# Performance work log

Hardware: AMD Instinct MI355X
Metric: run time of the kernel (lower is better)

## Reference

```python
import jax, jax.numpy as jnp
import numpy as np

B, N, D = 1024, 32, 512  # graphs, node types (=nodes per graph), node_dim
EPS = 1e-5

def setup_inputs() -> dict:
    key = jax.random.key(0)
    ks = jax.random.split(key, 6)
    z = jax.random.normal(ks[0], (B, N, D), jnp.float32)
    # each graph contains every node type exactly once, in random order
    idx = jax.vmap(lambda k: jax.random.permutation(k, N))(jax.random.split(ks[1], B)).astype(jnp.int32)
    A = jax.random.normal(ks[2], (N, N), jnp.float32) / np.sqrt(N)
    W1 = jax.random.normal(ks[3], (N, D, 2 * D), jnp.float32) / np.sqrt(D)
    b1 = jnp.zeros((N, 2 * D), jnp.float32)
    W2 = jax.random.normal(ks[4], (N, 2 * D, D), jnp.float32) / np.sqrt(2 * D)
    b2 = jnp.zeros((N, D), jnp.float32)
    gamma = jnp.ones((D,), jnp.float32)
    beta = jnp.zeros((D,), jnp.float32)
    return dict(z=z, idx=idx, A=A, W1=W1, b1=b1, W2=W2, b2=b2, gamma=gamma, beta=beta)

def _layernorm(x, g, b):
    m = jnp.mean(x, axis=-1, keepdims=True)
    v = jnp.var(x, axis=-1, keepdims=True)
    return (x - m) * jax.lax.rsqrt(v + EPS) * g + b

def reference(z, idx, A, W1, b1, W2, b2, gamma, beta):
    # per-graph submatrix of global A: A_sub[b] = A[node_index, node_index]
    A_sub = A[idx[:, :, None], idx[:, None, :]]            # [B,K,K]
    # Az[b] = A_sub[b].T @ z[b]
    Az = jnp.einsum('bkj,bkd->bjd', A_sub, z)              # [B,K,D]
    Az = _layernorm(Az, gamma, beta)
    # route node of type t to expert t: inv[b,t] = position of type t in graph b
    inv = jnp.argsort(idx, axis=1)                         # [B,N]
    x = jnp.take_along_axis(Az, inv[:, :, None], axis=1)   # [B,N,D] type-ordered
    # per-type 2-layer MLP experts (Linear -> ELU -> Linear), dropout in eval mode
    h = jax.nn.elu(jnp.einsum('bnd,ndh->bnh', x, W1) + b1) # [B,N,2D]
    y = jnp.einsum('bnh,nhd->bnd', h, W2) + b2             # [B,N,D]
    # scatter back to node order: node j in graph b has type idx[b,j]
    mix = jnp.take_along_axis(y, idx[:, :, None].astype(jnp.int32), axis=1)
    return mix + Az
```

## Files before the change

kernel.cpp:

```cpp
#include <hip/hip_runtime.h>
#include <hip/hip_bf16.h>
#include <math.h>

#define B_  1024
#define N_  32
#define D_  512
#define EPS_ 1e-5f

typedef __attribute__((ext_vector_type(8))) short bf16x8;
typedef __attribute__((ext_vector_type(4))) float f32x4;
using bf16 = __hip_bfloat16;
typedef unsigned int u32;
typedef const u32 __attribute__((address_space(1)))* gp_t;
typedef u32 __attribute__((address_space(3)))* sp_t;

static __device__ __forceinline__ void gload16(const void* g, void* s) {
  __builtin_amdgcn_global_load_lds((gp_t)g, (sp_t)s, 16, 0, 0);
}
static __device__ __forceinline__ void bar() {
  asm volatile("s_barrier" ::: "memory");
}

static __device__ __forceinline__ unsigned short f2bf(float f) {
  union { float f; u32 u; } c; c.f = f;
  u32 r = c.u + 0x7fff + ((c.u >> 16) & 1);
  return (unsigned short)(r >> 16);
}
static __device__ __forceinline__ float bf2f(unsigned short h) {
  union { u32 u; float f; } c; c.u = ((u32)h) << 16;
  return c.f;
}

static __device__ __forceinline__ void transpose_tile(
    const float* __restrict__ in, bf16* __restrict__ out,
    int R, int C, int bx, int by, int bz, int t) {
  __shared__ unsigned short tile[64][65];
  const size_t mat = (size_t)bz * (size_t)R * (size_t)C;
  const float* inp = in + mat;
  bf16* outp = out + mat;
  const int c0 = bx * 64, r0 = by * 64;
  const int tr = t >> 4;
  const int tc = (t & 15) * 4;
#pragma unroll
  for (int i = 0; i < 4; ++i) {
    const int r = tr + i * 16;
    float4 v = *(const float4*)&inp[(size_t)(r0 + r) * C + c0 + tc];
    tile[r][tc + 0] = f2bf(v.x);
    tile[r][tc + 1] = f2bf(v.y);
    tile[r][tc + 2] = f2bf(v.z);
    tile[r][tc + 3] = f2bf(v.w);
  }
  __syncthreads();
#pragma unroll
  for (int i = 0; i < 2; ++i) {
    const int chunk = i * 256 + t;
    const int c = chunk >> 3, r8 = (chunk & 7) * 8;
    union { bf16x8 v; unsigned short u[8]; } pk;
#pragma unroll
    for (int k = 0; k < 8; ++k) pk.u[k] = tile[r8 + k][c];
    *(bf16x8*)&outp[(size_t)(c0 + c) * R + r0 + r8] = pk.v;
  }
}

static __device__ __forceinline__ void mix_ln_body(
    int b, int t,
    const float* __restrict__ z, const int* __restrict__ idx,
    const float* __restrict__ A, const float* __restrict__ gamma,
    const float* __restrict__ beta, bf16* __restrict__ x_ws,
    int* __restrict__ inv_ws) {
  __shared__ float As[32][32];
  __shared__ int   p[32];
  __shared__ float red1[4][32];
  __shared__ float red2[4][32];
  __shared__ float meanS[32];
  __shared__ float rstdS[32];

  const int lane = t & 63, wid = t >> 6;
  const int llo = lane & 15, lhi = lane >> 4;

  if (t < 32) {
    int v = idx[b * 32 + t];
    p[t] = v;
    inv_ws[b * 32 + v] = t;
  }
  __syncthreads();
#pragma unroll
  for (int i = 0; i < 4; ++i) {
    const int id = i * 256 + t;
    As[id >> 5][id & 31] = A[p[id >> 5] * 32 + (id & 31)];
  }
  __syncthreads();

  bf16x8 af[2];
#pragma unroll
  for (int nt = 0; nt < 2; ++nt) {
    union { bf16x8 v; unsigned short s[8]; } u;
#pragma unroll
    for (int j = 0; j < 8; ++j)
      u.s[j] = f2bf(As[lhi * 8 + j][nt * 16 + llo]);
    af[nt] = u.v;
  }

  const float* zb = z + (size_t)b * (N_ * D_) + (size_t)(lhi * 8) * D_ + llo;
  const f32x4 fz = {0.f, 0.f, 0.f, 0.f};
  f32x4 acc[2][8];
#pragma unroll
  for (int nt = 0; nt < 2; ++nt)
#pragma unroll
    for (int dt = 0; dt < 8; ++dt) acc[nt][dt] = fz;

#pragma unroll
  for (int h = 0; h < 2; ++h) {
    float zr[4][8];
#pragma unroll
    for (int dd = 0; dd < 4; ++dd)
#pragma unroll
      for (int j = 0; j < 8; ++j)
        zr[dd][j] = zb[j * D_ + ((wid * 8 + h * 4 + dd) * 16)];
#pragma unroll
    for (int dd = 0; dd < 4; ++dd) {
      const int dt = h * 4 + dd;
      union { bf16x8 v; unsigned short s[8]; } u;
#pragma unroll
      for (int j = 0; j < 8; ++j) u.s[j] = f2bf(zr[dd][j]);
      acc[0][dt] = __builtin_amdgcn_mfma_f32_16x16x32_bf16(af[0], u.v, acc[0][dt], 0, 0, 0);
      acc[1][dt] = __builtin_amdgcn_mfma_f32_16x16x32_bf16(af[1], u.v, acc[1][dt], 0, 0, 0);
    }
  }

  float s1[2][4], s2[2][4];
#pragma unroll
  for (int nt = 0; nt < 2; ++nt)
#pragma unroll
    for (int r = 0; r < 4; ++r) {
      float a = 0.f, q = 0.f;
#pragma unroll
      for (int dt = 0; dt < 8; ++dt) {
        float v = acc[nt][dt][r];
        a += v; q += v * v;
      }
#pragma unroll
      for (int mk = 1; mk < 16; mk <<= 1) {
        a += __shfl_xor(a, mk);
        q += __shfl_xor(q, mk);
      }
      s1[nt][r] = a; s2[nt][r] = q;
    }
  if (llo == 0) {
#pragma unroll
    for (int nt = 0; nt < 2; ++nt)
#pragma unroll
      for (int r = 0; r < 4; ++r) {
        const int n = nt * 16 + lhi * 4 + r;
        red1[wid][n] = s1[nt][r];
        red2[wid][n] = s2[nt][r];
      }
  }
  __syncthreads();
  if (t < 32) {
    float S1 = red1[0][t] + red1[1][t] + red1[2][t] + red1[3][t];
    float S2 = red2[0][t] + red2[1][t] + red2[2][t] + red2[3][t];
    float mean = S1 * (1.f / D_);
    float var  = S2 * (1.f / D_) - mean * mean;
    meanS[t] = mean;
    rstdS[t] = rsqrtf(var + EPS_);
  }
  __syncthreads();

  float gv[8], bev[8];
#pragma unroll
  for (int dt = 0; dt < 8; ++dt) {
    const int d = (wid * 8 + dt) * 16 + llo;
    gv[dt] = gamma[d]; bev[dt] = beta[d];
  }
#pragma unroll
  for (int nt = 0; nt < 2; ++nt)
#pragma unroll
    for (int r = 0; r < 4; ++r) {
      const int n = nt * 16 + lhi * 4 + r;
      const float mn = meanS[n], rs = rstdS[n];
      unsigned short* xrow = (unsigned short*)(x_ws + ((size_t)n * B_ + b) * D_);
#pragma unroll
      for (int dt = 0; dt < 8; ++dt) {
        const int d = (wid * 8 + dt) * 16 + llo;
        float v = (acc[nt][dt][r] - mn) * rs * gv[dt] + bev[dt];
        xrow[d] = f2bf(v);
      }
    }
}

__global__ __launch_bounds__(256) void prep_kernel(
    const float* __restrict__ W1, const float* __restrict__ W2,
    bf16* __restrict__ W1t, bf16* __restrict__ W2t,
    const float* __restrict__ z, const int* __restrict__ idx,
    const float* __restrict__ A, const float* __restrict__ gamma,
    const float* __restrict__ beta, bf16* __restrict__ x_ws,
    int* __restrict__ inv_ws) {
  const int bid = blockIdx.x;
  const int t = threadIdx.x;
  if (bid < 4096) {
    transpose_tile(W1, W1t, 512, 1024, bid & 15, (bid >> 4) & 7, bid >> 7, t);
  } else if (bid < 8192) {
    const int b2 = bid - 4096;
    transpose_tile(W2, W2t, 1024, 512, b2 & 7, (b2 >> 3) & 15, b2 >> 7, t);
  } else {
    mix_ln_body(bid - 8192, t, z, idx, A, gamma, beta, x_ws, inv_ws);
  }
}

#define STGA(P, H, S)                                                         \
  gload16(Ag + (size_t)((H) * 128) * KD + (S) * 32 + soff,                    \
          lds + (P) * 16384 + (H) * 8192 + dof)
#define STGB(P, H, S)                                                         \
  gload16(Bg + (size_t)((H) * 128) * KD + (S) * 32 + soff,                    \
          lds + 32768 + (P) * 16384 + (H) * 8192 + dof)

#define RDA(P, H, AV) do {                                                    \
    const char* a_ = lds + (P) * 16384 + (H) * 8192;                          \
    AV[0] = *(const bf16x8*)(a_ + (widA * 32 + llo) * 64 + kx);               \
    AV[1] = *(const bf16x8*)(a_ + (widA * 32 + 16 + llo) * 64 + kx);          \
  } while (0)
#define RDB(P, H, BV) do {                                                    \
    const char* b_ = lds + 32768 + (P) * 16384 + (H) * 8192;                  \
    _Pragma("unroll")                                                         \
    for (int fj = 0; fj < 4; ++fj)                                            \
      BV[fj] = *(const bf16x8*)(b_ + (widB * 64 + fj * 16 + llo) * 64 + kx);  \
  } while (0)

#define MMA8(QR, QC, AV, BV) do {                                             \
    __builtin_amdgcn_s_setprio(1);                                            \
    _Pragma("unroll")                                                         \
    for (int fi = 0; fi < 2; ++fi)                                            \
      _Pragma("unroll")                                                       \
      for (int fj = 0; fj < 4; ++fj)                                          \
        acc[QR][QC][fi][fj] = __builtin_amdgcn_mfma_f32_16x16x32_bf16(        \
            AV[fi], BV[fj], acc[QR][QC][fi][fj], 0, 0, 0);                    \
    __builtin_amdgcn_s_setprio(0);                                            \
  } while (0)

#define VMC0() asm volatile("s_waitcnt vmcnt(0)" ::: "memory")

#define SUBTILE(P, S) do {                                                    \
    bf16x8 av[2], bv0[4], bv1[4];                                             \
    RDA(P, 0, av); RDB(P, 0, bv0); RDB(P, 1, bv1);                            \
    MMA8(0, 0, av, bv0);                                                      \
    MMA8(0, 1, av, bv1);                                                      \
    RDA(P, 1, av);                                                            \
    MMA8(1, 0, av, bv0);                                                      \
    MMA8(1, 1, av, bv1);                                                      \
    VMC0();                                  \
    bar();                                  \
    if ((S) + 2 < NS) {                                                       \
      STGA(P, 0, (S) + 2); STGA(P, 1, (S) + 2);                               \
      STGB(P, 0, (S) + 2); STGB(P, 1, (S) + 2);                               \
    }                                                                         \
  } while (0)

template <int KD, int NS>
static __device__ __forceinline__ void gemm_core(
    const bf16* __restrict__ Ag, const bf16* __restrict__ Bg,
    char* __restrict__ lds, f32x4 (&acc)[2][2][2][4], const int t) {
  const int lane = t & 63, wid = t >> 6;
  const int llo = lane & 15, lhi = lane >> 4;
  const int widA = wid & 3, widB = wid >> 2;
  const int kx = (lhi ^ ((llo >> 1) & 3)) * 16;
  const size_t soff = (size_t)(t >> 2) * KD + (size_t)(((t & 3) ^ ((t >> 3) & 3))) * 8;
  const int dof = wid * 1024;

  STGA(0, 0, 0); STGA(0, 1, 0); STGB(0, 0, 0); STGB(0, 1, 0);
  STGA(1, 0, 1); STGA(1, 1, 1); STGB(1, 0, 1); STGB(1, 1, 1);
  VMC0();
  bar();

#pragma unroll 1
  for (int it = 0; it < NS / 2; ++it) {
    SUBTILE(0, 2 * it);
    SUBTILE(1, 2 * it + 1);
  }
}

#define EPI(QC) do {                                                          \
    __syncthreads();                                                          \
    _Pragma("unroll")                                                         \
    for (int qr = 0; qr < 2; ++qr)                                            \
      _Pragma("unroll")                                                       \
      for (int fi = 0; fi < 2; ++fi) {                                        \
        const int h_loc = qr * 128 + (wid & 3) * 32 + fi * 16 + lhi * 4;      \
        const float4 bi = *(const float4*)&b1m[h_loc];                        \
        _Pragma("unroll")                                                     \
        for (int fj = 0; fj < 4; ++fj) {                                      \
          const int b_loc = (wid >> 2) * 64 + fj * 16 + llo;                  \
          float v0 = acc[qr][QC][fi][fj][0] + bi.x;                           \
          float v1 = acc[qr][QC][fi][fj][1] + bi.y;                           \
          float v2 = acc[qr][QC][fi][fj][2] + bi.z;                           \
          float v3 = acc[qr][QC][fi][fj][3] + bi.w;                           \
          v0 = v0 > 0.f ? v0 : __expf(v0) - 1.0f;                             \
          v1 = v1 > 0.f ? v1 : __expf(v1) - 1.0f;                             \
          v2 = v2 > 0.f ? v2 : __expf(v2) - 1.0f;                             \
          v3 = v3 > 0.f ? v3 : __expf(v3) - 1.0f;                             \
          ushort4 pk;                                                         \
          pk.x = f2bf(v0); pk.y = f2bf(v1); pk.z = f2bf(v2); pk.w = f2bf(v3); \
          const int byte = (b_loc * 512 + h_loc * 2) ^ ((b_loc & 7) << 4);    \
          *(ushort4*)(lds + byte) = pk;                                       \
        }                                                                     \
      }                                                                       \
    __syncthreads();                                                          \
    _Pragma("unroll")                                                         \
    for (int i = 0; i < 8; ++i) {                                             \
      const int c = i * 512 + t;                                              \
      const int bl = c >> 5, hc = c & 31;                                     \
      const int byte = (bl * 512 + hc * 16) ^ ((bl & 7) << 4);                \
      bf16x8 v = *(const bf16x8*)(lds + byte);                                \
      *(bf16x8*)&Hm[(size_t)(b0 + (QC) * 128 + bl) * 1024 + h0 + hc * 8] = v; \
    }                                                                         \
  } while (0)

__global__ __launch_bounds__(512, 2) void gemm1_kernel(
    const bf16* __restrict__ X,
    const bf16* __restrict__ W1t,
    const float* __restrict__ b1,
    bf16* __restrict__ Hout) {
  extern __shared__ char lds[];

  const int bid = blockIdx.x;
  const int swz = (bid & 7) * 64 + (bid >> 3);
  const int m  = swz >> 4;
  const int r_ = swz & 15;
  const int hb = r_ >> 2, bb = r_ & 3;

  const int t = threadIdx.x;
  const int lane = t & 63, wid = t >> 6;
  const int llo = lane & 15, lhi = lane >> 4;

  const bf16* Ag = W1t + (size_t)m * (1024 * 512) + (size_t)(hb * 256) * 512;
  const bf16* Bg = X   + (size_t)m * (1024 * 512) + (size_t)(bb * 256) * 512;

  const f32x4 fzero = {0.f, 0.f, 0.f, 0.f};
  f32x4 acc[2][2][2][4];
#pragma unroll
  for (int a = 0; a < 2; ++a)
#pragma unroll
    for (int b = 0; b < 2; ++b)
#pragma unroll
      for (int c = 0; c < 2; ++c)
#pragma unroll
        for (int d = 0; d < 4; ++d) acc[a][b][c][d] = fzero;

  gemm_core<512, 16>(Ag, Bg, lds, acc, t);

  bf16* Hm = Hout + (size_t)m * (1024 * 1024);
  const float* b1m = b1 + m * 1024 + hb * 256;
  const int b0 = bb * 256, h0 = hb * 256;
  EPI(0);
  EPI(1);
}

__global__ __launch_bounds__(512, 2) void gemm2_kernel(
    const bf16* __restrict__ Hin,
    const bf16* __restrict__ W2t,
    const float* __restrict__ b2,
    const bf16* __restrict__ Xb,
    const int* __restrict__ inv,
    float* __restrict__ out) {
  extern __shared__ char lds[];

  const int bid = blockIdx.x;
  const int swz = (bid & 7) * 32 + (bid >> 3);
  const int m  = swz >> 3;
  const int r_ = swz & 7;
  const int db_ = r_ >> 2, bb = r_ & 3;

  const int t = threadIdx.x;
  const int lane = t & 63, wid = t >> 6;
  const int llo = lane & 15, lhi = lane >> 4;

  const bf16* Ag = W2t + (size_t)m * (512 * 1024) + (size_t)(db_ * 256) * 1024;
  const bf16* Bg = Hin + (size_t)m * (1024 * 1024) + (size_t)(bb * 256) * 1024;

  const f32x4 fzero = {0.f, 0.f, 0.f, 0.f};
  f32x4 acc[2][2][2][4];
#pragma unroll
  for (int a = 0; a < 2; ++a)
#pragma unroll
    for (int b = 0; b < 2; ++b)
#pragma unroll
      for (int c = 0; c < 2; ++c)
#pragma unroll
        for (int d = 0; d < 4; ++d) acc[a][b][c][d] = fzero;

  gemm_core<1024, 32>(Ag, Bg, lds, acc, t);

  const float* b2m = b2 + m * 512;
  const bf16* Xm = Xb + (size_t)m * (1024 * 512);
#pragma unroll
  for (int qc = 0; qc < 2; ++qc)
#pragma unroll
    for (int fj = 0; fj < 4; ++fj) {
      const int b_ = bb * 256 + qc * 128 + (wid >> 2) * 64 + fj * 16 + llo;
      const int n_out = inv[b_ * 32 + m];
      float* orow = out + ((size_t)b_ * 32 + n_out) * 512;
      const bf16* xrow = Xm + (size_t)b_ * 512;
#pragma unroll
      for (int qr = 0; qr < 2; ++qr)
#pragma unroll
        for (int fi = 0; fi < 2; ++fi) {
          const int d0 = db_ * 256 + qr * 128 + (wid & 3) * 32 + fi * 16 + lhi * 4;
          const float4 bi = *(const float4*)&b2m[d0];
          const ushort4 xr = *(const ushort4*)&xrow[d0];
          float4 v;
          v.x = acc[qr][qc][fi][fj][0] + bi.x + bf2f(xr.x);
          v.y = acc[qr][qc][fi][fj][1] + bi.y + bf2f(xr.y);
          v.z = acc[qr][qc][fi][fj][2] + bi.z + bf2f(xr.z);
          v.w = acc[qr][qc][fi][fj][3] + bi.w + bf2f(xr.w);
          *(float4*)&orow[d0] = v;
        }
    }
}

extern "C" void kernel_launch(void* const* d_in, const int* in_sizes, int n_in,
                              void* d_out, int out_size, void* d_ws, size_t ws_size,
                              hipStream_t stream) {
  const float* z     = (const float*)d_in[0];
  const int*   idx   = (const int*)d_in[1];
  const float* A     = (const float*)d_in[2];
  const float* W1    = (const float*)d_in[3];
  const float* b1    = (const float*)d_in[4];
  const float* W2    = (const float*)d_in[5];
  const float* b2    = (const float*)d_in[6];
  const float* gamma = (const float*)d_in[7];
  const float* beta  = (const float*)d_in[8];
  float* out = (float*)d_out;
  char* ws = (char*)d_ws;

  const size_t OFF_X   = 0;
  const size_t OFF_H   = 33554432;
  const size_t OFF_W1T = 100663296;
  const size_t OFF_W2T = 134217728;
  const size_t OFF_INV = 167772160;
  const size_t NEED    = 167903232;
  if (ws_size < NEED) return;

  bf16* Xb  = (bf16*)(ws + OFF_X);
  bf16* Hb  = (bf16*)(ws + OFF_H);
  bf16* W1t = (bf16*)(ws + OFF_W1T);
  bf16* W2t = (bf16*)(ws + OFF_W2T);
  int*  inv = (int*)(ws + OFF_INV);

  hipFuncSetAttribute((const void*)gemm1_kernel,
                      hipFuncAttributeMaxDynamicSharedMemorySize, 65536);
  hipFuncSetAttribute((const void*)gemm2_kernel,
                      hipFuncAttributeMaxDynamicSharedMemorySize, 65536);

  prep_kernel<<<dim3(9216), 256, 0, stream>>>(W1, W2, W1t, W2t,
                                              z, idx, A, gamma, beta, Xb, inv);

  gemm1_kernel<<<dim3(512), 512, 65536, stream>>>(Xb, W1t, b1, Hb);
  gemm2_kernel<<<dim3(256), 512, 65536, stream>>>(Hb, W2t, b2, Xb, inv, out);
}
```

Measured before the change: 161.4 us.

## Retile gemm2 to 256x128 output tiles with smaller LDS footprint

Gemm2 is rewritten to compute 256x128 output tiles instead of 256x256, doubling the block count to 512 and shrinking dynamic LDS to 48KB. A dedicated staging/MFMA loop with a 4x4 fragment accumulator per wave replaces the shared gemm_core. The goal is more blocks per CU and better latency hiding and load balance. The cost is lower reuse of the W2 tile and more global traffic per FLOP.

```diff
diff --git a/kernel.cpp b/kernel.cpp
--- a/kernel.cpp
+++ b/kernel.cpp
@@ -248,8 +248,8 @@
     RDA(P, 1, av);                                                            \
     MMA8(1, 0, av, bv0);                                                      \
     MMA8(1, 1, av, bv1);                                                      \
-    VMC0();                                  \
-    bar();                                  \
+    VMC0();                                                                   \
+    bar();                                                                    \
     if ((S) + 2 < NS) {                                                       \
       STGA(P, 0, (S) + 2); STGA(P, 1, (S) + 2);                               \
       STGB(P, 0, (S) + 2); STGB(P, 1, (S) + 2);                               \
@@ -355,6 +355,43 @@
   EPI(1);
 }
 
+#define STGA2(P, H, S)                                                        \
+  gload16(Ag + (size_t)((H) * 128) * 1024 + (S) * 32 + soff,                  \
+          lds + (P) * 16384 + (H) * 8192 + dof)
+#define STGB2(P, S)                                                           \
+  gload16(Bg + (size_t)(S) * 32 + soff, lds + 32768 + (P) * 8192 + dof)
+
+#define RDA2(P, AV) do {                                                      \
+    const char* a_ = lds + (P) * 16384;                                       \
+    _Pragma("unroll")                                                         \
+    for (int fi = 0; fi < 4; ++fi)                                            \
+      AV[fi] = *(const bf16x8*)(a_ + (widA * 64 + fi * 16 + llo) * 64 + kx);  \
+  } while (0)
+#define RDB2(P, BV) do {                                                      \
+    const char* b_ = lds + 32768 + (P) * 8192;                                \
+    _Pragma("unroll")                                                         \
+    for (int fj = 0; fj < 4; ++fj)                                            \
+      BV[fj] = *(const bf16x8*)(b_ + (widB * 64 + fj * 16 + llo) * 64 + kx);  \
+  } while (0)
+
+#define SUBTILE2(P, S) do {                                                   \
+    bf16x8 av[4], bv[4];                                                      \
+    RDA2(P, av); RDB2(P, bv);                                                 \
+    __builtin_amdgcn_s_setprio(1);                                            \
+    _Pragma("unroll")                                                         \
+    for (int fi = 0; fi < 4; ++fi)                                            \
+      _Pragma("unroll")                                                       \
+      for (int fj = 0; fj < 4; ++fj)                                          \
+        acc[fi][fj] = __builtin_amdgcn_mfma_f32_16x16x32_bf16(                \
+            av[fi], bv[fj], acc[fi][fj], 0, 0, 0);                            \
+    __builtin_amdgcn_s_setprio(0);                                            \
+    VMC0();                                                                   \
+    bar();                                                                    \
+    if ((S) + 2 < 32) {                                                       \
+      STGA2(P, 0, (S) + 2); STGA2(P, 1, (S) + 2); STGB2(P, (S) + 2);          \
+    }                                                                         \
+  } while (0)
+
 __global__ __launch_bounds__(512, 2) void gemm2_kernel(
     const bf16* __restrict__ Hin,
     const bf16* __restrict__ W2t,
@@ -365,56 +402,61 @@
   extern __shared__ char lds[];
 
   const int bid = blockIdx.x;
-  const int swz = (bid & 7) * 32 + (bid >> 3);
-  const int m  = swz >> 3;
-  const int r_ = swz & 7;
-  const int db_ = r_ >> 2, bb = r_ & 3;
+  const int swz = (bid & 7) * 64 + (bid >> 3);
+  const int m  = swz >> 4;
+  const int r_ = swz & 15;
+  const int db_ = r_ >> 3, bb = r_ & 7;
 
   const int t = threadIdx.x;
   const int lane = t & 63, wid = t >> 6;
   const int llo = lane & 15, lhi = lane >> 4;
+  const int widA = wid & 3, widB = wid >> 2;
+  const int kx = (lhi ^ ((llo >> 1) & 3)) * 16;
+  const size_t soff = (size_t)(t >> 2) * 1024 + (size_t)(((t & 3) ^ ((t >> 3) & 3))) * 8;
+  const int dof = wid * 1024;
 
   const bf16* Ag = W2t + (size_t)m * (512 * 1024) + (size_t)(db_ * 256) * 1024;
-  const bf16* Bg = Hin + (size_t)m * (1024 * 1024) + (size_t)(bb * 256) * 1024;
+  const bf16* Bg = Hin + (size_t)m * (1024 * 1024) + (size_t)(bb * 128) * 1024;
 
   const f32x4 fzero = {0.f, 0.f, 0.f, 0.f};
-  f32x4 acc[2][2][2][4];
-#pragma unroll
-  for (int a = 0; a < 2; ++a)
-#pragma unroll
-    for (int b = 0; b < 2; ++b)
-#pragma unroll
-      for (int c = 0; c < 2; ++c)
-#pragma unroll
-        for (int d = 0; d < 4; ++d) acc[a][b][c][d] = fzero;
-
-  gemm_core<1024, 32>(Ag, Bg, lds, acc, t);
+  f32x4 acc[4][4];
+#pragma unroll
+  for (int a = 0; a < 4; ++a)
+#pragma unroll
+    for (int b = 0; b < 4; ++b) acc[a][b] = fzero;
+
+  STGA2(0, 0, 0); STGA2(0, 1, 0); STGB2(0, 0);
+  STGA2(1, 0, 1); STGA2(1, 1, 1); STGB2(1, 1);
+  VMC0();
+  bar();
+
+#pragma unroll 1
+  for (int it = 0; it < 16; ++it) {
+    SUBTILE2(0, 2 * it);
+    SUBTILE2(1, 2 * it + 1);
+  }
 
   const float* b2m = b2 + m * 512;
   const bf16* Xm = Xb + (size_t)m * (1024 * 512);
 #pragma unroll
-  for (int qc = 0; qc < 2; ++qc)
-#pragma unroll
-    for (int fj = 0; fj < 4; ++fj) {
-      const int b_ = bb * 256 + qc * 128 + (wid >> 2) * 64 + fj * 16 + llo;
-      const int n_out = inv[b_ * 32 + m];
-      float* orow = out + ((size_t)b_ * 32 + n_out) * 512;
-      const bf16* xrow = Xm + (size_t)b_ * 512;
-#pragma unroll
-      for (int qr = 0; qr < 2; ++qr)
-#pragma unroll
-        for (int fi = 0; fi < 2; ++fi) {
-          const int d0 = db_ * 256 + qr * 128 + (wid & 3) * 32 + fi * 16 + lhi * 4;
-          const float4 bi = *(const float4*)&b2m[d0];
-          const ushort4 xr = *(const ushort4*)&xrow[d0];
-          float4 v;
-          v.x = acc[qr][qc][fi][fj][0] + bi.x + bf2f(xr.x);
-          v.y = acc[qr][qc][fi][fj][1] + bi.y + bf2f(xr.y);
-          v.z = acc[qr][qc][fi][fj][2] + bi.z + bf2f(xr.z);
-          v.w = acc[qr][qc][fi][fj][3] + bi.w + bf2f(xr.w);
-          *(float4*)&orow[d0] = v;
-        }
+  for (int fj = 0; fj < 4; ++fj) {
+    const int b_ = bb * 128 + widB * 64 + fj * 16 + llo;
+    const int n_out = inv[b_ * 32 + m];
+    float* orow = out + ((size_t)b_ * 32 + n_out) * 512;
+    const bf16* xrow = Xm + (size_t)b_ * 512;
+#pragma unroll
+    for (int fi = 0; fi < 4; ++fi) {
+      const int d0 = db_ * 256 + widA * 64 + fi * 16 + lhi * 4;
+      const float4 bi = *(const float4*)&b2m[d0];
+      const ushort4 xr = *(const ushort4*)&xrow[d0];
+      float4 v;
+      v.x = acc[fi][fj][0] + bi.x + bf2f(xr.x);
+      v.y = acc[fi][fj][1] + bi.y + bf2f(xr.y);
+      v.z = acc[fi][fj][2] + bi.z + bf2f(xr.z);
+      v.w = acc[fi][fj][3] + bi.w + bf2f(xr.w);
+      *(float4*)&orow[d0] = v;
     }
+  }
 }
 
 extern "C" void kernel_launch(void* const* d_in, const int* in_sizes, int n_in,
@@ -449,11 +491,11 @@
   hipFuncSetAttribute((const void*)gemm1_kernel,
                       hipFuncAttributeMaxDynamicSharedMemorySize, 65536);
   hipFuncSetAttribute((const void*)gemm2_kernel,
-                      hipFuncAttributeMaxDynamicSharedMemorySize, 65536);
+                      hipFuncAttributeMaxDynamicSharedMemorySize, 49152);
 
   prep_kernel<<<dim3(9216), 256, 0, stream>>>(W1, W2, W1t, W2t,
                                               z, idx, A, gamma, beta, Xb, inv);
 
   gemm1_kernel<<<dim3(512), 512, 65536, stream>>>(Xb, W1t, b1, Hb);
-  gemm2_kernel<<<dim3(256), 512, 65536, stream>>>(Hb, W2t, b2, Xb, inv, out);
-}
+  gemm2_kernel<<<dim3(512), 512, 49152, stream>>>(Hb, W2t, b2, Xb, inv, out);
+}
```

Result: slower. 165.5 us (+2.5%).
